# Kernel tuning notes

Measured on AMD Instinct MI355X. Metric: run time of the kernel, lower is better.

## Reference

```python
import jax, jax.numpy as jnp
import numpy as np

N, E = 50000, 1_600_000
IN, HID, OUT = 2048, 64, 64


def setup_inputs() -> dict:
    key = jax.random.key(0)
    k1, k2, k3, k4 = jax.random.split(key, 4)
    x = jax.random.normal(k1, (N, IN), dtype=jnp.float32)
    edge_index = jax.random.randint(k2, (2, E), 0, N, dtype=jnp.int64)
    W1 = jax.random.normal(k3, (IN, HID), dtype=jnp.float32) / np.sqrt(IN)
    b1 = jnp.zeros((HID,), dtype=jnp.float32)
    W2 = jax.random.normal(k4, (HID, OUT), dtype=jnp.float32) / np.sqrt(HID)
    b2 = jnp.zeros((OUT,), dtype=jnp.float32)
    return {"x": x, "edge_index": edge_index, "W1": W1, "b1": b1, "W2": W2, "b2": b2}


def gcn_conv(x, edge_index, W, b):
    # PyG GCNConv: h = XW; out = D^{-1/2} (A + I) D^{-1/2} h + b
    n = x.shape[0]
    h = x @ W  # [n, d_out]
    loops = jnp.arange(n, dtype=edge_index.dtype)
    src = jnp.concatenate([edge_index[0], loops])  # [E+n]
    dst = jnp.concatenate([edge_index[1], loops])
    deg = jax.ops.segment_sum(jnp.ones_like(dst, dtype=h.dtype), dst, num_segments=n)
    dinv = jax.lax.rsqrt(deg)  # deg >= 1 because of self-loops
    norm = dinv[src] * dinv[dst]  # [E+n]
    out = jax.ops.segment_sum(h[src] * norm[:, None], dst, num_segments=n)
    return out + b


def reference(x, edge_index, W1, b1, W2, b2):
    h = jax.nn.relu(gcn_conv(x, edge_index, W1, b1))
    h = jax.nn.relu(gcn_conv(h, edge_index, W2, b2))
    return h.mean(axis=0)  # [OUT]
```

## Files before the change

kernel.cpp:

```cpp
#include <hip/hip_runtime.h>
#include <hip/hip_bf16.h>

typedef __attribute__((ext_vector_type(8))) short short8_t;
typedef __attribute__((ext_vector_type(4))) float f32x4;

__device__ __forceinline__ short f2bf(float x){
  union { float f; unsigned u; } v; v.f = x;
  unsigned r = v.u + 0x7fffu + ((v.u >> 16) & 1u);
  return (short)(r >> 16);
}
__device__ __forceinline__ unsigned pack2(float lo, float hi){
  return (unsigned)(unsigned short)f2bf(lo) | ((unsigned)(unsigned short)f2bf(hi) << 16);
}
__device__ __forceinline__ float bf2f(unsigned short u){
  union { unsigned u; float f; } v; v.u = ((unsigned)u) << 16; return v.f;
}

__global__ __launch_bounds__(256) void k_wconv2(const float* __restrict__ W1, short* __restrict__ Wb1,
                                                const float* __restrict__ W2, short* __restrict__ Wb2){
  int tid = blockIdx.x*256 + threadIdx.x;
  const float* W; short* Wb; int t;
  if (tid < 64*2048){ W = W1; Wb = Wb1; t = tid; }
  else if (tid < 64*2048 + 2*2048){ W = W2; Wb = Wb2; t = tid - 64*2048; }
  else return;
  int e  = t & 7;
  int l  = (t >> 3) & 63;
  int nt = (t >> 9) & 3;
  int kt = t >> 11;
  int k  = kt*32 + (l >> 4)*8 + e;
  int col = nt*16 + (l & 15);
  Wb[t] = f2bf(W[(size_t)k*64 + col]);
}

__global__ __launch_bounds__(256) void k_hist_gemm1(const int* __restrict__ ei, int* __restrict__ cnt,
                                                    int* __restrict__ rank, int E,
                                                    const float* __restrict__ A, const short* __restrict__ Wb,
                                                    float* __restrict__ h1raw, int M, int HB){
  __shared__ unsigned short lds[4*16*256];
  int b = blockIdx.x;
  int tid = threadIdx.x;
  if (b & 1){
    for (int i = (b>>1)*256 + tid; i < E; i += HB*256)
      rank[i] = atomicAdd(&cnt[ei[E + i]], 1);
    return;
  }
  int g = b >> 1;
  int wid = tid >> 6, lane = tid & 63;
  int tile = wid >> 1, kh = wid & 1;
  int row0 = g*32 + tile*16;
  int rfrag = lane & 15, grp = lane >> 4;
  char* ldsb = (char*)lds;
  const short8_t* wb = (const short8_t*)Wb + lane;
  f32x4 acc0 = {0.f,0.f,0.f,0.f}, acc1 = acc0, acc2 = acc0, acc3 = acc0;

  int wbase = wid*16*512;
  int wsel  = (lane >> 1);
  int whalf = (lane & 1) << 3;

  for (int ko = 0; ko < 4; ++ko){
    int kcol = kh*1024 + ko*256;
    #pragma unroll
    for (int r = 0; r < 16; ++r){
      int rowc = row0 + r; if (rowc >= M) rowc = M - 1;
      const float4 a = *(const float4*)(A + (size_t)rowc*2048 + kcol + lane*4);
      uint2 p; p.x = pack2(a.x, a.y); p.y = pack2(a.z, a.w);
      *(uint2*)(ldsb + wbase + r*512 + ((wsel ^ (r & 7)) << 4) + whalf) = p;
    }
    asm volatile("s_waitcnt lgkmcnt(0)" ::: "memory");
    #pragma unroll
    for (int kt = 0; kt < 8; ++kt){
      short8_t af = *(const short8_t*)(ldsb + wbase + rfrag*512 + ((((kt<<2) + grp) ^ (rfrag & 7)) << 4));
      int ktg = kh*32 + ko*8 + kt;
      short8_t b0 = wb[(ktg*4+0)*64];
      short8_t b1 = wb[(ktg*4+1)*64];
      short8_t b2 = wb[(ktg*4+2)*64];
      short8_t b3 = wb[(ktg*4+3)*64];
      acc0 = __builtin_amdgcn_mfma_f32_16x16x32_bf16(af, b0, acc0, 0,0,0);
      acc1 = __builtin_amdgcn_mfma_f32_16x16x32_bf16(af, b1, acc1, 0,0,0);
      acc2 = __builtin_amdgcn_mfma_f32_16x16x32_bf16(af, b2, acc2, 0,0,0);
      acc3 = __builtin_amdgcn_mfma_f32_16x16x32_bf16(af, b3, acc3, 0,0,0);
    }
  }

  if (kh == 1){
    float* xch = (float*)(ldsb + wbase);
    *(f32x4*)(xch + lane*20 +  0) = acc0;
    *(f32x4*)(xch + lane*20 +  4) = acc1;
    *(f32x4*)(xch + lane*20 +  8) = acc2;
    *(f32x4*)(xch + lane*20 + 12) = acc3;
  }
  __syncthreads();
  if (kh == 1) return;
  {
    float* px = (float*)(ldsb + (wid+1)*16*512);
    acc0 += *(const f32x4*)(px + lane*20 +  0);
    acc1 += *(const f32x4*)(px + lane*20 +  4);
    acc2 += *(const f32x4*)(px + lane*20 +  8);
    acc3 += *(const f32x4*)(px + lane*20 + 12);
  }

  int orow = row0 + grp*4;
  float* op = h1raw + (size_t)orow*64 + rfrag;
  #pragma unroll
  for (int reg = 0; reg < 4; ++reg){
    if (orow + reg < M){
      op[reg*64 +  0] = acc0[reg];
      op[reg*64 + 16] = acc1[reg];
      op[reg*64 + 32] = acc2[reg];
      op[reg*64 + 48] = acc3[reg];
    }
  }
}

__global__ __launch_bounds__(256) void k_part(const int* __restrict__ cnt, int* __restrict__ partial, int N){
  int b = blockIdx.x, t = threadIdx.x;
  int chunk = (N + 255) >> 8;
  int lo = b*chunk, hi = lo + chunk; if (hi > N) hi = N;
  int s = 0;
  for (int i = lo + t; i < hi; i += 256) s += cnt[i];
  __shared__ int sm[256];
  sm[t] = s; __syncthreads();
  for (int d = 128; d; d >>= 1){ if (t < d) sm[t] += sm[t+d]; __syncthreads(); }
  if (t == 0) partial[b] = sm[0];
}

__global__ __launch_bounds__(256) void k_scan2(const int* __restrict__ cnt, const int* __restrict__ partial,
                                               int* __restrict__ off, float* __restrict__ dinv, int N){
  int b = blockIdx.x, t = threadIdx.x;
  __shared__ int ps[256];
  ps[t] = partial[t]; __syncthreads();
  for (int d = 1; d < 256; d <<= 1){
    int v = (t >= d) ? ps[t-d] : 0; __syncthreads(); ps[t] += v; __syncthreads();
  }
  int base  = b ? ps[b-1] : 0;
  int total = ps[255];
  int chunk = (N + 255) >> 8;
  int lo = b*chunk, hi = lo + chunk; if (hi > N) hi = N;
  __shared__ int vs[256];
  int run = base;
  for (int j0 = lo; j0 < hi; j0 += 256){
    int i = j0 + t;
    int c = (i < hi) ? cnt[i] : 0;
    vs[t] = c; __syncthreads();
    for (int d = 1; d < 256; d <<= 1){
      int v = (t >= d) ? vs[t-d] : 0; __syncthreads(); vs[t] += v; __syncthreads();
    }
    if (i < hi){
      off[i] = run + vs[t] - c;
      dinv[i] = rsqrtf((float)(c + 1));
    }
    run += vs[255];
    __syncthreads();
  }
  if (b == 255 && t == 0) off[N] = total;
}

__global__ __launch_bounds__(256) void k_scatter_scale(const int* __restrict__ ei, const int* __restrict__ off,
                                                       const int* __restrict__ rank, int* __restrict__ ebuf, int E,
                                                       const float* __restrict__ h1raw, const float* __restrict__ dinv,
                                                       unsigned short* __restrict__ h1, int total8, int EB){
  if ((int)blockIdx.x < EB){
    int i = blockIdx.x*256 + threadIdx.x;
    if (i < E){
      int s = ei[i], d = ei[E + i];
      ebuf[off[d] + rank[i]] = s;
    }
    return;
  }
  int t = (blockIdx.x - EB)*256 + threadIdx.x;
  if (t >= total8) return;
  int base = t*8;
  float dv = dinv[base >> 6];
  const float4 a0 = *(const float4*)(h1raw + base);
  const float4 a1 = *(const float4*)(h1raw + base + 4);
  short8_t o;
  o[0]=f2bf(a0.x*dv); o[1]=f2bf(a0.y*dv); o[2]=f2bf(a0.z*dv); o[3]=f2bf(a0.w*dv);
  o[4]=f2bf(a1.x*dv); o[5]=f2bf(a1.y*dv); o[6]=f2bf(a1.z*dv); o[7]=f2bf(a1.w*dv);
  *(short8_t*)(h1 + base) = o;
}

template<int KTILES>
__global__ __launch_bounds__(256) void k_gemm_sm(const unsigned short* __restrict__ Ah,
                                                 const short* __restrict__ Wb, const float* __restrict__ dinv,
                                                 unsigned short* __restrict__ out, int M, int lda){
  int wid = threadIdx.x >> 6, lane = threadIdx.x & 63;
  int row0 = (blockIdx.x*4 + wid)*16;
  if (row0 >= M) return;
  int r = lane & 15, g = lane >> 4;
  const short8_t* wb = (const short8_t*)Wb + lane;
  f32x4 acc0 = {0.f,0.f,0.f,0.f}, acc1 = acc0, acc2 = acc0, acc3 = acc0;
  #pragma unroll
  for (int kt = 0; kt < KTILES; ++kt){
    short8_t af = *(const short8_t*)(Ah + (size_t)(row0 + r)*lda + kt*32 + g*8);
    short8_t b0 = wb[(kt*4+0)*64];
    short8_t b1 = wb[(kt*4+1)*64];
    short8_t b2 = wb[(kt*4+2)*64];
    short8_t b3 = wb[(kt*4+3)*64];
    acc0 = __builtin_amdgcn_mfma_f32_16x16x32_bf16(af, b0, acc0, 0,0,0);
    acc1 = __builtin_amdgcn_mfma_f32_16x16x32_bf16(af, b1, acc1, 0,0,0);
    acc2 = __builtin_amdgcn_mfma_f32_16x16x32_bf16(af, b2, acc2, 0,0,0);
    acc3 = __builtin_amdgcn_mfma_f32_16x16x32_bf16(af, b3, acc3, 0,0,0);
  }
  int orow = row0 + g*4;
  float d0 = dinv[orow], d1 = dinv[orow+1], d2 = dinv[orow+2], d3 = dinv[orow+3];
  unsigned short* op = out + (size_t)orow*64 + r;
  op[0*64 +  0] = (unsigned short)f2bf(acc0[0]*d0);
  op[0*64 + 16] = (unsigned short)f2bf(acc1[0]*d0);
  op[0*64 + 32] = (unsigned short)f2bf(acc2[0]*d0);
  op[0*64 + 48] = (unsigned short)f2bf(acc3[0]*d0);
  op[1*64 +  0] = (unsigned short)f2bf(acc0[1]*d1);
  op[1*64 + 16] = (unsigned short)f2bf(acc1[1]*d1);
  op[1*64 + 32] = (unsigned short)f2bf(acc2[1]*d1);
  op[1*64 + 48] = (unsigned short)f2bf(acc3[1]*d1);
  op[2*64 +  0] = (unsigned short)f2bf(acc0[2]*d2);
  op[2*64 + 16] = (unsigned short)f2bf(acc1[2]*d2);
  op[2*64 + 32] = (unsigned short)f2bf(acc2[2]*d2);
  op[2*64 + 48] = (unsigned short)f2bf(acc3[2]*d2);
  op[3*64 +  0] = (unsigned short)f2bf(acc0[3]*d3);
  op[3*64 + 16] = (unsigned short)f2bf(acc1[3]*d3);
  op[3*64 + 32] = (unsigned short)f2bf(acc2[3]*d3);
  op[3*64 + 48] = (unsigned short)f2bf(acc3[3]*d3);
}

template<bool FUSE>
__global__ __launch_bounds__(256) void k_agg(const unsigned short* __restrict__ hin, const int* __restrict__ off,
                                             const int* __restrict__ ebuf, const float* __restrict__ dinv,
                                             const float* __restrict__ bias, void* __restrict__ outp, int N){
  int lane = threadIdx.x & 63, wid = threadIdx.x >> 6;
  float b = bias[lane];
  float fsum = 0.f;
  int stride = gridDim.x*4;
  for (int i = blockIdx.x*4 + wid; i < N; i += stride){
    float acc = bf2f(hin[(size_t)i*64 + lane]);
    int j  = off[i];
    int j1 = off[i+1];
    for (; j + 4 <= j1; j += 4){
      int s0 = ebuf[j], s1 = ebuf[j+1], s2 = ebuf[j+2], s3 = ebuf[j+3];
      acc += bf2f(hin[(size_t)s0*64 + lane]);
      acc += bf2f(hin[(size_t)s1*64 + lane]);
      acc += bf2f(hin[(size_t)s2*64 + lane]);
      acc += bf2f(hin[(size_t)s3*64 + lane]);
    }
    for (; j < j1; ++j){
      int s = ebuf[j];
      acc += bf2f(hin[(size_t)s*64 + lane]);
    }
    float z = fmaxf(dinv[i]*acc + b, 0.f);
    if (FUSE) fsum += z;
    else ((unsigned short*)outp)[(size_t)i*64 + lane] = (unsigned short)f2bf(z);
  }
  if (FUSE){
    __shared__ float sm[4][64];
    sm[wid][lane] = fsum;
    __syncthreads();
    if (wid == 0)
      ((float*)outp)[(size_t)blockIdx.x*64 + lane] = sm[0][lane] + sm[1][lane] + sm[2][lane] + sm[3][lane];
  }
}

__global__ __launch_bounds__(256) void k_final(const float* __restrict__ part, float* __restrict__ out,
                                               int NB, float invN){
  int f = blockIdx.x;
  float s = 0.f;
  for (int b = threadIdx.x; b < NB; b += 256) s += part[(size_t)b*64 + f];
  __shared__ float sm[256];
  sm[threadIdx.x] = s; __syncthreads();
  for (int d = 128; d > 0; d >>= 1){
    if (threadIdx.x < d) sm[threadIdx.x] += sm[threadIdx.x + d];
    __syncthreads();
  }
  if (threadIdx.x == 0) out[f] = sm[0]*invN;
}

extern "C" void kernel_launch(void* const* d_in, const int* in_sizes, int n_in,
                              void* d_out, int out_size, void* d_ws, size_t ws_size,
                              hipStream_t stream){
  const float* x  = (const float*)d_in[0];
  const int*   ei = (const int*)d_in[1];
  const float* W1 = (const float*)d_in[2];
  const float* b1 = (const float*)d_in[3];
  const float* W2 = (const float*)d_in[4];
  const float* b2 = (const float*)d_in[5];
  float* out = (float*)d_out;

  const int IN = 2048;
  int N = in_sizes[0] / IN;
  int E = in_sizes[1] / 2;

  char* w = (char*)d_ws;
  auto alloc = [&](size_t bytes){ char* p = w; w += (bytes + 255) & ~255ULL; return (void*)p; };
  int*   cnt     = (int*)  alloc((size_t)N*4);
  int*   off     = (int*)  alloc((size_t)(N+1)*4);
  float* dinv    = (float*)alloc((size_t)N*4);
  int*   partial = (int*)  alloc(256*4);
  int*   rank    = (int*)  alloc((size_t)E*4);
  int*   ebuf    = (int*)  alloc((size_t)E*4);
  short* Wb1     = (short*)alloc((size_t)64*2048*2);
  short* Wb2     = (short*)alloc((size_t)2*2048*2);
  float* h1raw   = (float*)alloc((size_t)N*64*4);
  unsigned short* h1 = (unsigned short*)alloc((size_t)N*64*2);
  unsigned short* z1 = (unsigned short*)alloc((size_t)N*64*2);
  const int NB2 = 2048;
  float* part    = (float*)alloc((size_t)NB2*64*4);

  int EB = (E + 255)/256;
  int GB = (N + 31)/32;
  int HB = GB;
  int total8 = N*8;
  int SB = (total8 + 255)/256;
  int smblocks = ((N + 15)/16 + 3)/4;

  hipMemsetAsync(cnt, 0, (size_t)N*4, stream);
  k_wconv2 <<<(64*2048 + 2*2048 + 255)/256, 256, 0, stream>>>(W1, Wb1, W2, Wb2);
  k_hist_gemm1<<<2*GB, 256, 0, stream>>>(ei, cnt, rank, E, x, Wb1, h1raw, N, HB);
  k_part   <<<256, 256, 0, stream>>>(cnt, partial, N);
  k_scan2  <<<256, 256, 0, stream>>>(cnt, partial, off, dinv, N);
  k_scatter_scale<<<EB + SB, 256, 0, stream>>>(ei, off, rank, ebuf, E, h1raw, dinv, h1, total8, EB);
  k_agg<false><<<NB2, 256, 0, stream>>>(h1, off, ebuf, dinv, b1, (void*)z1, N);
  k_gemm_sm<2><<<smblocks, 256, 0, stream>>>(z1, Wb2, dinv, h1, N, 64);
  k_agg<true> <<<NB2, 256, 0, stream>>>(h1, off, ebuf, dinv, b2, (void*)part, N);
  k_final  <<<64, 256, 0, stream>>>(part, out, NB2, 1.0f/(float)N);
}
```

Measured before the change: 397.5 us.

## Move source-degree scaling into aggregation and write GEMM1 output as bf16

GEMM1 now stores bf16 directly instead of an fp32 intermediate. The separate dinv pre-scale pass is removed, and its work moves into the aggregation kernels, which gather dinv[src] per edge. The histogram atomics now run inside each GEMM block after its tile is finished, instead of in interleaved separate blocks. This removes an fp32 round trip of N*64 values and one elementwise pass, at the cost of an extra random dinv gather per edge in both aggregations.

```diff
diff --git a/kernel.cpp b/kernel.cpp
--- a/kernel.cpp
+++ b/kernel.cpp
@@ -32,22 +32,16 @@
   Wb[t] = f2bf(W[(size_t)k*64 + col]);
 }
 
-__global__ __launch_bounds__(256) void k_hist_gemm1(const int* __restrict__ ei, int* __restrict__ cnt,
-                                                    int* __restrict__ rank, int E,
-                                                    const float* __restrict__ A, const short* __restrict__ Wb,
-                                                    float* __restrict__ h1raw, int M, int HB){
+__global__ __launch_bounds__(256) void k_gemm1_hist(const float* __restrict__ A, const short* __restrict__ Wb,
+                                                    unsigned short* __restrict__ h1, int M,
+                                                    const int* __restrict__ ei, int* __restrict__ cnt,
+                                                    int* __restrict__ rank, int E, int GB){
   __shared__ unsigned short lds[4*16*256];
   int b = blockIdx.x;
   int tid = threadIdx.x;
-  if (b & 1){
-    for (int i = (b>>1)*256 + tid; i < E; i += HB*256)
-      rank[i] = atomicAdd(&cnt[ei[E + i]], 1);
-    return;
-  }
-  int g = b >> 1;
   int wid = tid >> 6, lane = tid & 63;
   int tile = wid >> 1, kh = wid & 1;
-  int row0 = g*32 + tile*16;
+  int row0 = b*32 + tile*16;
   int rfrag = lane & 15, grp = lane >> 4;
   char* ldsb = (char*)lds;
   const short8_t* wb = (const short8_t*)Wb + lane;
@@ -90,26 +84,30 @@
     *(f32x4*)(xch + lane*20 + 12) = acc3;
   }
   __syncthreads();
-  if (kh == 1) return;
-  {
+  if (kh == 0){
     float* px = (float*)(ldsb + (wid+1)*16*512);
     acc0 += *(const f32x4*)(px + lane*20 +  0);
     acc1 += *(const f32x4*)(px + lane*20 +  4);
     acc2 += *(const f32x4*)(px + lane*20 +  8);
     acc3 += *(const f32x4*)(px + lane*20 + 12);
-  }
-
-  int orow = row0 + grp*4;
-  float* op = h1raw + (size_t)orow*64 + rfrag;
-  #pragma unroll
-  for (int reg = 0; reg < 4; ++reg){
-    if (orow + reg < M){
-      op[reg*64 +  0] = acc0[reg];
-      op[reg*64 + 16] = acc1[reg];
-      op[reg*64 + 32] = acc2[reg];
-      op[reg*64 + 48] = acc3[reg];
-    }
-  }
+
+    int orow = row0 + grp*4;
+    unsigned short* op = h1 + (size_t)orow*64 + rfrag;
+    #pragma unroll
+    for (int reg = 0; reg < 4; ++reg){
+      if (orow + reg < M){
+        op[reg*64 +  0] = (unsigned short)f2bf(acc0[reg]);
+        op[reg*64 + 16] = (unsigned short)f2bf(acc1[reg]);
+        op[reg*64 + 32] = (unsigned short)f2bf(acc2[reg]);
+        op[reg*64 + 48] = (unsigned short)f2bf(acc3[reg]);
+      }
+    }
+  }
+
+  int per = (E + GB - 1)/GB;
+  int lo = b*per, hi = lo + per; if (hi > E) hi = E;
+  for (int i = lo + tid; i < hi; i += 256)
+    rank[i] = atomicAdd(&cnt[ei[E + i]], 1);
 }
 
 __global__ __launch_bounds__(256) void k_part(const int* __restrict__ cnt, int* __restrict__ partial, int N){
@@ -155,33 +153,18 @@
   if (b == 255 && t == 0) off[N] = total;
 }
 
-__global__ __launch_bounds__(256) void k_scatter_scale(const int* __restrict__ ei, const int* __restrict__ off,
-                                                       const int* __restrict__ rank, int* __restrict__ ebuf, int E,
-                                                       const float* __restrict__ h1raw, const float* __restrict__ dinv,
-                                                       unsigned short* __restrict__ h1, int total8, int EB){
-  if ((int)blockIdx.x < EB){
-    int i = blockIdx.x*256 + threadIdx.x;
-    if (i < E){
-      int s = ei[i], d = ei[E + i];
-      ebuf[off[d] + rank[i]] = s;
-    }
-    return;
-  }
-  int t = (blockIdx.x - EB)*256 + threadIdx.x;
-  if (t >= total8) return;
-  int base = t*8;
-  float dv = dinv[base >> 6];
-  const float4 a0 = *(const float4*)(h1raw + base);
-  const float4 a1 = *(const float4*)(h1raw + base + 4);
-  short8_t o;
-  o[0]=f2bf(a0.x*dv); o[1]=f2bf(a0.y*dv); o[2]=f2bf(a0.z*dv); o[3]=f2bf(a0.w*dv);
-  o[4]=f2bf(a1.x*dv); o[5]=f2bf(a1.y*dv); o[6]=f2bf(a1.z*dv); o[7]=f2bf(a1.w*dv);
-  *(short8_t*)(h1 + base) = o;
+__global__ __launch_bounds__(256) void k_scatter(const int* __restrict__ ei, const int* __restrict__ off,
+                                                 const int* __restrict__ rank, int* __restrict__ ebuf, int E){
+  int i = blockIdx.x*256 + threadIdx.x;
+  if (i < E){
+    int s = ei[i], d = ei[E + i];
+    ebuf[off[d] + rank[i]] = s;
+  }
 }
 
 template<int KTILES>
 __global__ __launch_bounds__(256) void k_gemm_sm(const unsigned short* __restrict__ Ah,
-                                                 const short* __restrict__ Wb, const float* __restrict__ dinv,
+                                                 const short* __restrict__ Wb,
                                                  unsigned short* __restrict__ out, int M, int lda){
   int wid = threadIdx.x >> 6, lane = threadIdx.x & 63;
   int row0 = (blockIdx.x*4 + wid)*16;
@@ -202,24 +185,14 @@
     acc3 = __builtin_amdgcn_mfma_f32_16x16x32_bf16(af, b3, acc3, 0,0,0);
   }
   int orow = row0 + g*4;
-  float d0 = dinv[orow], d1 = dinv[orow+1], d2 = dinv[orow+2], d3 = dinv[orow+3];
   unsigned short* op = out + (size_t)orow*64 + r;
-  op[0*64 +  0] = (unsigned short)f2bf(acc0[0]*d0);
-  op[0*64 + 16] = (unsigned short)f2bf(acc1[0]*d0);
-  op[0*64 + 32] = (unsigned short)f2bf(acc2[0]*d0);
-  op[0*64 + 48] = (unsigned short)f2bf(acc3[0]*d0);
-  op[1*64 +  0] = (unsigned short)f2bf(acc0[1]*d1);
-  op[1*64 + 16] = (unsigned short)f2bf(acc1[1]*d1);
-  op[1*64 + 32] = (unsigned short)f2bf(acc2[1]*d1);
-  op[1*64 + 48] = (unsigned short)f2bf(acc3[1]*d1);
-  op[2*64 +  0] = (unsigned short)f2bf(acc0[2]*d2);
-  op[2*64 + 16] = (unsigned short)f2bf(acc1[2]*d2);
-  op[2*64 + 32] = (unsigned short)f2bf(acc2[2]*d2);
-  op[2*64 + 48] = (unsigned short)f2bf(acc3[2]*d2);
-  op[3*64 +  0] = (unsigned short)f2bf(acc0[3]*d3);
-  op[3*64 + 16] = (unsigned short)f2bf(acc1[3]*d3);
-  op[3*64 + 32] = (unsigned short)f2bf(acc2[3]*d3);
-  op[3*64 + 48] = (unsigned short)f2bf(acc3[3]*d3);
+  #pragma unroll
+  for (int reg = 0; reg < 4; ++reg){
+    op[reg*64 +  0] = (unsigned short)f2bf(acc0[reg]);
+    op[reg*64 + 16] = (unsigned short)f2bf(acc1[reg]);
+    op[reg*64 + 32] = (unsigned short)f2bf(acc2[reg]);
+    op[reg*64 + 48] = (unsigned short)f2bf(acc3[reg]);
+  }
 }
 
 template<bool FUSE>
@@ -231,21 +204,23 @@
   float fsum = 0.f;
   int stride = gridDim.x*4;
   for (int i = blockIdx.x*4 + wid; i < N; i += stride){
-    float acc = bf2f(hin[(size_t)i*64 + lane]);
+    float di = dinv[i];
+    float acc = di*bf2f(hin[(size_t)i*64 + lane]);
     int j  = off[i];
     int j1 = off[i+1];
     for (; j + 4 <= j1; j += 4){
       int s0 = ebuf[j], s1 = ebuf[j+1], s2 = ebuf[j+2], s3 = ebuf[j+3];
-      acc += bf2f(hin[(size_t)s0*64 + lane]);
-      acc += bf2f(hin[(size_t)s1*64 + lane]);
-      acc += bf2f(hin[(size_t)s2*64 + lane]);
-      acc += bf2f(hin[(size_t)s3*64 + lane]);
+      float w0 = dinv[s0], w1 = dinv[s1], w2 = dinv[s2], w3 = dinv[s3];
+      acc += w0*bf2f(hin[(size_t)s0*64 + lane]);
+      acc += w1*bf2f(hin[(size_t)s1*64 + lane]);
+      acc += w2*bf2f(hin[(size_t)s2*64 + lane]);
+      acc += w3*bf2f(hin[(size_t)s3*64 + lane]);
     }
     for (; j < j1; ++j){
       int s = ebuf[j];
-      acc += bf2f(hin[(size_t)s*64 + lane]);
-    }
-    float z = fmaxf(dinv[i]*acc + b, 0.f);
+      acc += dinv[s]*bf2f(hin[(size_t)s*64 + lane]);
+    }
+    float z = fmaxf(di*acc + b, 0.f);
     if (FUSE) fsum += z;
     else ((unsigned short*)outp)[(size_t)i*64 + lane] = (unsigned short)f2bf(z);
   }
@@ -297,7 +272,6 @@
   int*   ebuf    = (int*)  alloc((size_t)E*4);
   short* Wb1     = (short*)alloc((size_t)64*2048*2);
   short* Wb2     = (short*)alloc((size_t)2*2048*2);
-  float* h1raw   = (float*)alloc((size_t)N*64*4);
   unsigned short* h1 = (unsigned short*)alloc((size_t)N*64*2);
   unsigned short* z1 = (unsigned short*)alloc((size_t)N*64*2);
   const int NB2 = 2048;
@@ -305,19 +279,16 @@
 
   int EB = (E + 255)/256;
   int GB = (N + 31)/32;
-  int HB = GB;
-  int total8 = N*8;
-  int SB = (total8 + 255)/256;
   int smblocks = ((N + 15)/16 + 3)/4;
 
   hipMemsetAsync(cnt, 0, (size_t)N*4, stream);
   k_wconv2 <<<(64*2048 + 2*2048 + 255)/256, 256, 0, stream>>>(W1, Wb1, W2, Wb2);
-  k_hist_gemm1<<<2*GB, 256, 0, stream>>>(ei, cnt, rank, E, x, Wb1, h1raw, N, HB);
+  k_gemm1_hist<<<GB, 256, 0, stream>>>(x, Wb1, h1, N, ei, cnt, rank, E, GB);
   k_part   <<<256, 256, 0, stream>>>(cnt, partial, N);
   k_scan2  <<<256, 256, 0, stream>>>(cnt, partial, off, dinv, N);
-  k_scatter_scale<<<EB + SB, 256, 0, stream>>>(ei, off, rank, ebuf, E, h1raw, dinv, h1, total8, EB);
+  k_scatter<<<EB, 256, 0, stream>>>(ei, off, rank, ebuf, E);
   k_agg<false><<<NB2, 256, 0, stream>>>(h1, off, ebuf, dinv, b1, (void*)z1, N);
-  k_gemm_sm<2><<<smblocks, 256, 0, stream>>>(z1, Wb2, dinv, h1, N, 64);
+  k_gemm_sm<2><<<smblocks, 256, 0, stream>>>(z1, Wb2, h1, N, 64);
   k_agg<true> <<<NB2, 256, 0, stream>>>(h1, off, ebuf, dinv, b2, (void*)part, N);
   k_final  <<<64, 256, 0, stream>>>(part, out, NB2, 1.0f/(float)N);
 }
```

Result: faster. 363.3 us (-8.6%).
